# Optimization experiments

Hardware: AMD Instinct MI355X
Metric: run time of the kernel (lower is better)

## Reference

```python
import jax, jax.numpy as jnp
import numpy as np

# KWConv2d config: in=256, out=256, k=3, s=1, p=1, groups=1, bias=False
# warehouse: 32 spatial cells of shape [64, 64, 3, 3]; num_fourier_basis=0; temp_value=0
B, CIN, H, W_ = 32, 256, 56, 56
OUT = 256
NUM_CELLS, CO, CI, KH, KW = 32, 64, 64, 3, 3
HIDDEN = 16                 # max(int(256 * 0.0625), 16)
GO, GI, GS = OUT // CO, CIN // CI, 1
M = GO * GI * GS            # num_local_mixture = 16
P = NUM_CELLS + 1           # kw_planes_per_mixture = 33
KWP = P * M                 # kw_planes = 528


def setup_inputs() -> dict:
    key = jax.random.key(0)
    ks = jax.random.split(key, 4)
    s = 0.02
    return {
        "x": jax.random.normal(ks[0], (B, CIN, H, W_), jnp.float32),
        "cells": jax.random.normal(ks[1], (NUM_CELLS, CO, CI, KH, KW), jnp.float32) * s,
        "fc1_w": jax.random.normal(ks[2], (HIDDEN, CIN), jnp.float32) * s,
        "fc1_b": jnp.zeros((HIDDEN,), jnp.float32),
        "ln_g": jnp.ones((HIDDEN,), jnp.float32),
        "ln_b": jnp.zeros((HIDDEN,), jnp.float32),
        "sp_w": jax.random.normal(ks[3], (KWP, HIDDEN), jnp.float32) * s,
        "sp_b": jnp.zeros((KWP,), jnp.float32),
    }


def _attention(x, fc1_w, fc1_b, ln_g, ln_b, sp_w, sp_b):
    # AdaptiveAvgPool1d(1) over flattened spatial dims == global mean
    pooled = x.mean(axis=(2, 3))                      # [B, CIN]
    h = pooled @ fc1_w.T + fc1_b                      # [B, HIDDEN]
    mu = h.mean(-1, keepdims=True)
    var = ((h - mu) ** 2).mean(-1, keepdims=True)
    h = (h - mu) * jax.lax.rsqrt(var + 1e-5) * ln_g + ln_b
    h = jax.nn.relu(h)
    a = h @ sp_w.T + sp_b                             # spatial_head -> [B, KWP]
    a = a.reshape(-1, P)                              # [B*M, P]
    a = a / (jnp.abs(a).sum(axis=1, keepdims=True) + 0.001)  # L1 normalize per mixture
    # temp_value = 0 -> attention unchanged; drop last (zero) column
    return a[:, :-1]                                  # [B*M, NUM_CELLS]


def reference(x, cells, fc1_w, fc1_b, ln_g, ln_b, sp_w, sp_b):
    att = _attention(x, fc1_w, fc1_b, ln_g, ln_b, sp_w, sp_b)  # [B*M, NUM_CELLS]
    w = cells.reshape(NUM_CELLS, -1)                  # [NUM_CELLS, CO*CI*KH*KW]
    agg = att @ w                                     # [B*M, CO*CI*KH*KW]
    agg = agg.reshape(B, GS, GO, GI, CO, CI, KH, KW)
    agg = agg.transpose(0, 2, 4, 3, 5, 1, 6, 7)       # torch permute (0,2,4,3,5,1,6,7)
    agg = agg.reshape(B * OUT, CIN, KH, KW)           # per-sample kernels (groups=1)
    # grouped-conv trick: fold batch into channels, groups = B
    xr = x.reshape(1, B * CIN, H, W_)
    out = jax.lax.conv_general_dilated(
        xr, agg, window_strides=(1, 1), padding=((1, 1), (1, 1)),
        dimension_numbers=("NCHW", "OIHW", "NCHW"), feature_group_count=B)
    return out.reshape(B, OUT, H, W_)
```

## Files before the change

kernel.cpp:

```cpp
#include <hip/hip_runtime.h>
#include <stdint.h>

typedef unsigned short ush;
typedef __bf16   bf16x8 __attribute__((ext_vector_type(8)));
typedef float    f32x4  __attribute__((ext_vector_type(4)));
typedef uint32_t u32x4  __attribute__((ext_vector_type(4)));

union U16B { u32x4 u; bf16x8 b; };
union P8   { ush us[8]; u32x4 v; };

template<int V> struct ICx { static constexpr int value = V; };

__device__ __forceinline__ ush f2bf(float f) {
    union { float f; uint32_t u; } v; v.f = f;
    uint32_t r = v.u + 0x7FFFu + ((v.u >> 16) & 1u);
    return (ush)(r >> 16);
}

__device__ __forceinline__ void gl_lds16(const ush* g, ush* l) {
    __builtin_amdgcn_global_load_lds(
        (const __attribute__((address_space(1))) uint32_t*)g,
        (__attribute__((address_space(3))) uint32_t*)l, 16, 0, 0);
}

#define HWPX  3136
#define POOL_OFF   58720256UL
#define ATT_OFF    58753024UL
#define WAGG_OFF   58818560UL

__global__ void k_halo(u32x4* __restrict__ xT16, u32x4* __restrict__ pooled16) {
    int i = blockIdx.x * 256 + threadIdx.x;
    int rl = i >> 3, s = i & 7;
    u32x4 z = (u32x4)(0u);
    size_t byte = (size_t)rl * 4096 + (s < 4 ? s * 16 : 3648 + (s - 4) * 16);
    xT16[byte >> 4] = z;
    if (blockIdx.x < 8) pooled16[blockIdx.x * 256 + threadIdx.x] = z;
}

__global__ void k_transpose(const float* __restrict__ x, ush* __restrict__ xT,
                            float* __restrict__ pooled) {
    __shared__ float tile[64][65];
    int blk = blockIdx.x;
    int b   = blk / 196;
    int rem = blk % 196;
    int icg = rem / 49;
    int pxg = rem % 49;
    int t = threadIdx.x;

    {
        int icl  = t >> 2, part = t & 3;
        const float* src = x + (size_t)(b * 256 + icg * 64 + icl) * HWPX + pxg * 64 + part * 16;
        #pragma unroll
        for (int k = 0; k < 4; ++k) {
            f32x4 v = *(const f32x4*)(src + k * 4);
            tile[icl][part * 16 + k * 4 + 0] = v[0];
            tile[icl][part * 16 + k * 4 + 1] = v[1];
            tile[icl][part * 16 + k * 4 + 2] = v[2];
            tile[icl][part * 16 + k * 4 + 3] = v[3];
        }
    }
    __syncthreads();

    if (t < 64) {
        float s = 0.f;
        #pragma unroll 8
        for (int p = 0; p < 64; ++p) s += tile[t][p];
        atomicAdd(pooled + b * 256 + icg * 64 + t, s);
    }

    {
        int pxl = t >> 2, icq = t & 3;
        int px  = pxg * 64 + pxl;
        int row = px / 56;
        int col = px - row * 56;
        int p   = col + 1;
        int xorp = (p >> 1) & 3;
        int icg32   = icg * 2 + (icq >> 1);
        int subbase = (icq & 1) * 2;
        P8 lo, hi;
        #pragma unroll
        for (int m = 0; m < 8; ++m) {
            lo.us[m] = f2bf(tile[icq * 16 + m][pxl]);
            hi.us[m] = f2bf(tile[icq * 16 + 8 + m][pxl]);
        }
        size_t base = (((size_t)(b * 8 + icg32) * 56 + row) * 64 + p) * 32;
        *(u32x4*)(xT + base + (size_t)((subbase ^ xorp) * 8))       = lo.v;
        *(u32x4*)(xT + base + (size_t)(((subbase + 1) ^ xorp) * 8)) = hi.v;
    }
}

__global__ void k_attn(const float* __restrict__ pooled,
                       const float* __restrict__ fc1_w, const float* __restrict__ fc1_b,
                       const float* __restrict__ ln_g,  const float* __restrict__ ln_b,
                       const float* __restrict__ sp_w,  const float* __restrict__ sp_b,
                       float* __restrict__ att) {
    __shared__ float hs[32][16];
    int t = threadIdx.x;
    {
        int b = t >> 4, j = t & 15;
        float acc = 0.f;
        for (int c = 0; c < 256; ++c) acc += pooled[b * 256 + c] * fc1_w[j * 256 + c];
        hs[b][j] = fc1_b[j] + acc * (1.0f / 3136.0f);
    }
    __syncthreads();
    if (t < 32) {
        float mu = 0.f;
        #pragma unroll
        for (int j = 0; j < 16; ++j) mu += hs[t][j];
        mu *= (1.0f / 16.0f);
        float var = 0.f;
        #pragma unroll
        for (int j = 0; j < 16; ++j) { float d = hs[t][j] - mu; var += d * d; }
        var *= (1.0f / 16.0f);
        float inv = rsqrtf(var + 1e-5f);
        #pragma unroll
        for (int j = 0; j < 16; ++j) {
            float v = (hs[t][j] - mu) * inv * ln_g[j] + ln_b[j];
            hs[t][j] = fmaxf(v, 0.f);
        }
    }
    __syncthreads();
    {
        int b = t >> 4, m = t & 15;
        float a[33];
        #pragma unroll 1
        for (int i = 0; i < 33; ++i) {
            int p = m * 33 + i;
            float acc = sp_b[p];
            #pragma unroll
            for (int j = 0; j < 16; ++j) acc += hs[b][j] * sp_w[p * 16 + j];
            a[i] = acc;
        }
        float s = 0.f;
        #pragma unroll
        for (int i = 0; i < 33; ++i) s += fabsf(a[i]);
        float inv = 1.0f / (s + 0.001f);
        #pragma unroll
        for (int c = 0; c < 32; ++c) att[(b * 16 + m) * 32 + c] = a[c] * inv;
    }
}

__global__ void k_agg(const float* __restrict__ cells, const float* __restrict__ att,
                      ush* __restrict__ wagg) {
    __shared__ float at[512];
    int blk = blockIdx.x;
    int b = blk >> 6, co = blk & 63;
    int t = threadIdx.x;
    for (int i = t; i < 512; i += 256) at[i] = att[b * 512 + i];
    __syncthreads();
    int ci = t & 63, gi = t >> 6;
    float acc[4][9];
    #pragma unroll
    for (int g = 0; g < 4; ++g)
        #pragma unroll
        for (int k = 0; k < 9; ++k) acc[g][k] = 0.f;
    for (int c = 0; c < 32; ++c) {
        float a0 = at[(0 + gi) * 32 + c];
        float a1 = at[(4 + gi) * 32 + c];
        float a2 = at[(8 + gi) * 32 + c];
        float a3 = at[(12 + gi) * 32 + c];
        const float* cp = cells + (size_t)c * 36864 + co * 576 + ci * 9;
        #pragma unroll
        for (int k = 0; k < 9; ++k) {
            float cv = cp[k];
            acc[0][k] += a0 * cv; acc[1][k] += a1 * cv;
            acc[2][k] += a2 * cv; acc[3][k] += a3 * cv;
        }
    }
    #pragma unroll
    for (int g = 0; g < 4; ++g)
        #pragma unroll
        for (int k = 0; k < 9; ++k)
            wagg[((size_t)(b * 9 + k) * 256 + g * 64 + co) * 256 + gi * 64 + ci] = f2bf(acc[g][k]);
}

__global__ __launch_bounds__(256, 2) void k_conv(const ush* __restrict__ xT,
                                                 const ush* __restrict__ wagg,
                                                 float* __restrict__ out) {
    __shared__ __align__(16) ush xs[2][12288];

    int tid = threadIdx.x;
    int wg  = blockIdx.x;
    int xcd = wg & 7;
    int kk  = wg >> 3;
    int gq  = kk / 14;
    int sp  = kk - gq * 14;
    int g   = gq * 8 + xcd;
    int b   = g >> 1, octile = g & 1;
    int row0 = sp * 4, oc0 = octile * 128;

    int lane = tid & 63, w = tid >> 6;
    int wm = w >> 1, wn = w & 1;
    int l15 = lane & 15, s4 = lane >> 4;

    {
        u32x4 z = (u32x4)(0u);
        #pragma unroll
        for (int i = 0; i < 12; ++i) ((u32x4*)xs)[tid + i * 256] = z;
    }

    int prow[7], pq[7];
    #pragma unroll
    for (int j = 0; j < 7; ++j) {
        int px = wn * 112 + j * 16 + l15;
        prow[j] = px / 56;
        pq[j]   = px - prow[j] * 56;
    }

    unsigned vmask = 0;
    #pragma unroll
    for (int k = 0; k < 6; ++k) {
        int grow = row0 - 1 + k;
        if (grow >= 0 && grow < 56) vmask |= 1u << k;
    }

    const ush* wb = wagg + (size_t)b * 9 * 65536 + (size_t)(oc0 + wm * 64 + l15) * 256 + s4 * 8;
    const ush* xb = xT + (size_t)b * 8 * 56 * 2048 + (size_t)tid * 8;
    ush* lq = &xs[0][0];

    f32x4 acc[4][7];
    #pragma unroll
    for (int mi = 0; mi < 4; ++mi)
        #pragma unroll
        for (int j = 0; j < 7; ++j) acc[mi][j] = (f32x4)(0.f);

    U16B wpa[2][4];
    #pragma unroll
    for (int mi = 0; mi < 4; ++mi) {
        wpa[0][mi].u = *(const u32x4*)(wb + mi * 4096);
        wpa[1][mi].u = *(const u32x4*)(wb + 65536 + mi * 4096);
    }

    __syncthreads();

    #pragma unroll
    for (int k = 0; k < 6; ++k)
        if (vmask & (1u << k))
            gl_lds16(xb + (size_t)(row0 - 1 + k) * 2048, lq + k * 2048 + w * 512);
    __syncthreads();

    auto chunk_body = [&](auto parc, int chunk) {
        constexpr int PAR = decltype(parc)::value;
        if (chunk < 7) {
            #pragma unroll
            for (int k = 0; k < 6; ++k)
                if (vmask & (1u << k))
                    gl_lds16(xb + (size_t)((chunk + 1) * 56 + row0 - 1 + k) * 2048,
                             lq + (PAR ^ 1) * 12288 + k * 2048 + w * 512);
        }
        const ush* xsb = xs[PAR];
        #pragma unroll
        for (int tap = 0; tap < 9; ++tap) {
            const int dy = tap / 3, dx = tap % 3;
            U16B a0, a1, a2, a3;
            if ((PAR + tap) & 1) { a0 = wpa[1][0]; a1 = wpa[1][1]; a2 = wpa[1][2]; a3 = wpa[1][3]; }
            else                 { a0 = wpa[0][0]; a1 = wpa[0][1]; a2 = wpa[0][2]; a3 = wpa[0][3]; }
            {
                int nt = tap + 2, nc = chunk;
                if (nt >= 9) { nt -= 9; ++nc; }
                if (nc < 8) {
                    const ush* wnx = wb + (size_t)nt * 65536 + (size_t)nc * 32;
                    if ((PAR + tap) & 1) {
                        #pragma unroll
                        for (int mi = 0; mi < 4; ++mi) wpa[1][mi].u = *(const u32x4*)(wnx + mi * 4096);
                    } else {
                        #pragma unroll
                        for (int mi = 0; mi < 4; ++mi) wpa[0][mi].u = *(const u32x4*)(wnx + mi * 4096);
                    }
                }
            }
            #pragma unroll
            for (int j = 0; j < 7; ++j) {
                int q    = pq[j] + dx;
                int slot = s4 ^ ((q >> 1) & 3);
                int off  = ((prow[j] + dy) * 64 + q) * 32 + slot * 8;
                U16B bj; bj.u = *(const u32x4*)(xsb + off);
                acc[0][j] = __builtin_amdgcn_mfma_f32_16x16x32_bf16(bj.b, a0.b, acc[0][j], 0, 0, 0);
                acc[1][j] = __builtin_amdgcn_mfma_f32_16x16x32_bf16(bj.b, a1.b, acc[1][j], 0, 0, 0);
                acc[2][j] = __builtin_amdgcn_mfma_f32_16x16x32_bf16(bj.b, a2.b, acc[2][j], 0, 0, 0);
                acc[3][j] = __builtin_amdgcn_mfma_f32_16x16x32_bf16(bj.b, a3.b, acc[3][j], 0, 0, 0);
            }
        }
        __syncthreads();
    };

    for (int c2 = 0; c2 < 8; c2 += 2) {
        chunk_body(ICx<0>{}, c2);
        chunk_body(ICx<1>{}, c2 + 1);
    }

    int pxbase = row0 * 56 + wn * 112 + s4 * 4;
    #pragma unroll
    for (int mi = 0; mi < 4; ++mi) {
        int oc = oc0 + wm * 64 + mi * 16 + l15;
        float* o = out + (size_t)(b * 256 + oc) * HWPX + pxbase;
        #pragma unroll
        for (int j = 0; j < 7; ++j)
            *(f32x4*)(o + j * 16) = acc[mi][j];
    }
}

extern "C" void kernel_launch(void* const* d_in, const int* in_sizes, int n_in,
                              void* d_out, int out_size, void* d_ws, size_t ws_size,
                              hipStream_t stream) {
    const float* x     = (const float*)d_in[0];
    const float* cells = (const float*)d_in[1];
    const float* fc1_w = (const float*)d_in[2];
    const float* fc1_b = (const float*)d_in[3];
    const float* ln_g  = (const float*)d_in[4];
    const float* ln_b  = (const float*)d_in[5];
    const float* sp_w  = (const float*)d_in[6];
    const float* sp_b  = (const float*)d_in[7];
    float* out = (float*)d_out;

    char* ws = (char*)d_ws;
    ush*   xT     = (ush*)ws;
    float* pooled = (float*)(ws + POOL_OFF);
    float* att    = (float*)(ws + ATT_OFF);
    ush*   wagg   = (ush*)(ws + WAGG_OFF);

    k_halo<<<448, 256, 0, stream>>>((u32x4*)ws, (u32x4*)pooled);
    k_transpose<<<6272, 256, 0, stream>>>(x, xT, pooled);
    k_attn<<<1, 512, 0, stream>>>(pooled, fc1_w, fc1_b, ln_g, ln_b, sp_w, sp_b, att);
    k_agg<<<2048, 256, 0, stream>>>(cells, att, wagg);
    k_conv<<<896, 256, 0, stream>>>(xT, wagg, out);
}
```

Baseline: 275.8 us.

## Halve conv output-channel tile, stage weights in LDS, drop double buffering

The conv kernel now uses 64 output channels per workgroup instead of 128, and launches twice as many workgroups. Weight fragments are staged through padded, swizzled LDS for each input-channel chunk instead of being prefetched into registers from global memory. The double-buffered input tile becomes single-buffered, so loads no longer overlap compute. It also adds s_setprio around the MFMA bursts and a staggered s_sleep for half the workgroups, trading re-reading the input tile for each output-channel tile and lost prefetch overlap against fewer registers and more parallelism.

```diff
diff --git a/kernel.cpp b/kernel.cpp
--- a/kernel.cpp
+++ b/kernel.cpp
@@ -8,8 +8,6 @@
 
 union U16B { u32x4 u; bf16x8 b; };
 union P8   { ush us[8]; u32x4 v; };
-
-template<int V> struct ICx { static constexpr int value = V; };
 
 __device__ __forceinline__ ush f2bf(float f) {
     union { float f; uint32_t u; } v; v.f = f;
@@ -177,7 +175,8 @@
 __global__ __launch_bounds__(256, 2) void k_conv(const ush* __restrict__ xT,
                                                  const ush* __restrict__ wagg,
                                                  float* __restrict__ out) {
-    __shared__ __align__(16) ush xs[2][12288];
+    __shared__ __align__(16) ush xs[12288];
+    __shared__ __align__(16) ush wsh[23040];
 
     int tid = threadIdx.x;
     int wg  = blockIdx.x;
@@ -186,8 +185,8 @@
     int gq  = kk / 14;
     int sp  = kk - gq * 14;
     int g   = gq * 8 + xcd;
-    int b   = g >> 1, octile = g & 1;
-    int row0 = sp * 4, oc0 = octile * 128;
+    int b   = g >> 2, octile = g & 3;
+    int row0 = sp * 4, oc0 = octile * 64;
 
     int lane = tid & 63, w = tid >> 6;
     int wm = w >> 1, wn = w & 1;
@@ -196,7 +195,7 @@
     {
         u32x4 z = (u32x4)(0u);
         #pragma unroll
-        for (int i = 0; i < 12; ++i) ((u32x4*)xs)[tid + i * 256] = z;
+        for (int i = 0; i < 6; ++i) ((u32x4*)xs)[tid + i * 256] = z;
     }
 
     int prow[7], pq[7];
@@ -214,85 +213,62 @@
         if (grow >= 0 && grow < 56) vmask |= 1u << k;
     }
 
-    const ush* wb = wagg + (size_t)b * 9 * 65536 + (size_t)(oc0 + wm * 64 + l15) * 256 + s4 * 8;
+    const ush* wgl = wagg + (size_t)b * 9 * 65536 + (size_t)(oc0 + (tid >> 2)) * 256 + (tid & 3) * 8;
+    ush* wdst = wsh + (tid >> 2) * 40 + (((tid & 3) ^ ((tid >> 2) & 3)) * 8);
+    const ush* wrd = wsh + (wm * 32 + l15) * 40 + ((s4 ^ (l15 & 3)) * 8);
     const ush* xb = xT + (size_t)b * 8 * 56 * 2048 + (size_t)tid * 8;
-    ush* lq = &xs[0][0];
-
-    f32x4 acc[4][7];
-    #pragma unroll
-    for (int mi = 0; mi < 4; ++mi)
+
+    f32x4 acc[2][7];
+    #pragma unroll
+    for (int mi = 0; mi < 2; ++mi)
         #pragma unroll
         for (int j = 0; j < 7; ++j) acc[mi][j] = (f32x4)(0.f);
 
-    U16B wpa[2][4];
-    #pragma unroll
-    for (int mi = 0; mi < 4; ++mi) {
-        wpa[0][mi].u = *(const u32x4*)(wb + mi * 4096);
-        wpa[1][mi].u = *(const u32x4*)(wb + 65536 + mi * 4096);
-    }
-
-    __syncthreads();
-
-    #pragma unroll
-    for (int k = 0; k < 6; ++k)
-        if (vmask & (1u << k))
-            gl_lds16(xb + (size_t)(row0 - 1 + k) * 2048, lq + k * 2048 + w * 512);
-    __syncthreads();
-
-    auto chunk_body = [&](auto parc, int chunk) {
-        constexpr int PAR = decltype(parc)::value;
-        if (chunk < 7) {
-            #pragma unroll
-            for (int k = 0; k < 6; ++k)
-                if (vmask & (1u << k))
-                    gl_lds16(xb + (size_t)((chunk + 1) * 56 + row0 - 1 + k) * 2048,
-                             lq + (PAR ^ 1) * 12288 + k * 2048 + w * 512);
-        }
-        const ush* xsb = xs[PAR];
+    __syncthreads();
+
+    if ((kk >> 5) & 1) __builtin_amdgcn_s_sleep(32);
+
+    for (int cc = 0; cc < 8; ++cc) {
+        U16B wst[9];
+        const ush* wcg = wgl + (size_t)cc * 32;
+        #pragma unroll
+        for (int k = 0; k < 9; ++k) wst[k].u = *(const u32x4*)(wcg + (size_t)k * 65536);
+        #pragma unroll
+        for (int k = 0; k < 6; ++k)
+            if (vmask & (1u << k))
+                gl_lds16(xb + (size_t)(cc * 56 + row0 - 1 + k) * 2048, xs + k * 2048 + w * 512);
+        #pragma unroll
+        for (int k = 0; k < 9; ++k) *(u32x4*)(wdst + k * 2560) = wst[k].u;
+        __syncthreads();
+
         #pragma unroll
         for (int tap = 0; tap < 9; ++tap) {
             const int dy = tap / 3, dx = tap % 3;
-            U16B a0, a1, a2, a3;
-            if ((PAR + tap) & 1) { a0 = wpa[1][0]; a1 = wpa[1][1]; a2 = wpa[1][2]; a3 = wpa[1][3]; }
-            else                 { a0 = wpa[0][0]; a1 = wpa[0][1]; a2 = wpa[0][2]; a3 = wpa[0][3]; }
-            {
-                int nt = tap + 2, nc = chunk;
-                if (nt >= 9) { nt -= 9; ++nc; }
-                if (nc < 8) {
-                    const ush* wnx = wb + (size_t)nt * 65536 + (size_t)nc * 32;
-                    if ((PAR + tap) & 1) {
-                        #pragma unroll
-                        for (int mi = 0; mi < 4; ++mi) wpa[1][mi].u = *(const u32x4*)(wnx + mi * 4096);
-                    } else {
-                        #pragma unroll
-                        for (int mi = 0; mi < 4; ++mi) wpa[0][mi].u = *(const u32x4*)(wnx + mi * 4096);
-                    }
-                }
-            }
+            U16B wf0, wf1;
+            wf0.u = *(const u32x4*)(wrd + tap * 2560);
+            wf1.u = *(const u32x4*)(wrd + tap * 2560 + 16 * 40);
+            U16B bx[7];
             #pragma unroll
             for (int j = 0; j < 7; ++j) {
                 int q    = pq[j] + dx;
                 int slot = s4 ^ ((q >> 1) & 3);
-                int off  = ((prow[j] + dy) * 64 + q) * 32 + slot * 8;
-                U16B bj; bj.u = *(const u32x4*)(xsb + off);
-                acc[0][j] = __builtin_amdgcn_mfma_f32_16x16x32_bf16(bj.b, a0.b, acc[0][j], 0, 0, 0);
-                acc[1][j] = __builtin_amdgcn_mfma_f32_16x16x32_bf16(bj.b, a1.b, acc[1][j], 0, 0, 0);
-                acc[2][j] = __builtin_amdgcn_mfma_f32_16x16x32_bf16(bj.b, a2.b, acc[2][j], 0, 0, 0);
-                acc[3][j] = __builtin_amdgcn_mfma_f32_16x16x32_bf16(bj.b, a3.b, acc[3][j], 0, 0, 0);
+                bx[j].u = *(const u32x4*)(xs + ((prow[j] + dy) * 64 + q) * 32 + slot * 8);
             }
+            __builtin_amdgcn_s_setprio(1);
+            #pragma unroll
+            for (int j = 0; j < 7; ++j) {
+                acc[0][j] = __builtin_amdgcn_mfma_f32_16x16x32_bf16(bx[j].b, wf0.b, acc[0][j], 0, 0, 0);
+                acc[1][j] = __builtin_amdgcn_mfma_f32_16x16x32_bf16(bx[j].b, wf1.b, acc[1][j], 0, 0, 0);
+            }
+            __builtin_amdgcn_s_setprio(0);
         }
         __syncthreads();
-    };
-
-    for (int c2 = 0; c2 < 8; c2 += 2) {
-        chunk_body(ICx<0>{}, c2);
-        chunk_body(ICx<1>{}, c2 + 1);
     }
 
     int pxbase = row0 * 56 + wn * 112 + s4 * 4;
     #pragma unroll
-    for (int mi = 0; mi < 4; ++mi) {
-        int oc = oc0 + wm * 64 + mi * 16 + l15;
+    for (int mi = 0; mi < 2; ++mi) {
+        int oc = oc0 + wm * 32 + mi * 16 + l15;
         float* o = out + (size_t)(b * 256 + oc) * HWPX + pxbase;
         #pragma unroll
         for (int j = 0; j < 7; ++j)
@@ -323,5 +299,5 @@
     k_transpose<<<6272, 256, 0, stream>>>(x, xT, pooled);
     k_attn<<<1, 512, 0, stream>>>(pooled, fc1_w, fc1_b, ln_g, ln_b, sp_w, sp_b, att);
     k_agg<<<2048, 256, 0, stream>>>(cells, att, wagg);
-    k_conv<<<896, 256, 0, stream>>>(xT, wagg, out);
-}
+    k_conv<<<1792, 256, 0, stream>>>(xT, wagg, out);
+}
```

Measured after the change: 234.4 us. 1.18x faster.
